# Performance work log

Measured on AMD Instinct MI355X. Metric: run time of the kernel, lower is better.

## Reference

```python
import jax, jax.numpy as jnp
import numpy as np

VOCAB = 14
D_MODEL = 1024
D_FF = 4096
B, S = 8, 2048
EPS = 1e-5


def _linear_params(key, d_in, d_out):
    kw, kb = jax.random.split(key)
    lim = 1.0 / np.sqrt(d_in)
    W = jax.random.uniform(kw, (d_out, d_in), jnp.float32, -lim, lim)
    b = jax.random.uniform(kb, (d_out,), jnp.float32, -lim, lim)
    return W, b


def setup_inputs() -> dict:
    key = jax.random.key(0)
    ks = jax.random.split(key, 8)
    x = jax.random.randint(ks[0], (B, S), 0, VOCAB)
    tok_emb = jax.random.normal(ks[1], (VOCAB, D_MODEL), jnp.float32)
    qw, qb = _linear_params(ks[2], D_MODEL, D_MODEL)
    kw, kb = _linear_params(ks[3], D_MODEL, D_MODEL)
    vw, vb = _linear_params(ks[4], D_MODEL, D_MODEL)
    pw, pb = _linear_params(ks[5], D_MODEL, D_MODEL)
    f1w, f1b = _linear_params(ks[6], D_MODEL, D_FF)
    f2w, f2b = _linear_params(ks[7], D_FF, D_MODEL)
    ones = jnp.ones((D_MODEL,), jnp.float32)
    zeros = jnp.zeros((D_MODEL,), jnp.float32)
    return {
        "x": x, "tok_emb": tok_emb,
        "ln1_w": ones, "ln1_b": zeros,
        "qw": qw, "qb": qb, "kw": kw, "kb": kb, "vw": vw, "vb": vb,
        "pw": pw, "pb": pb,
        "ln2_w": ones, "ln2_b": zeros,
        "f1w": f1w, "f1b": f1b, "f2w": f2w, "f2b": f2b,
        "lnf_w": ones, "lnf_b": zeros,
    }


def _layernorm(h, w, b):
    mu = jnp.mean(h, axis=-1, keepdims=True)
    var = jnp.var(h, axis=-1, keepdims=True)
    return (h - mu) / jnp.sqrt(var + EPS) * w + b


def reference(x, tok_emb, ln1_w, ln1_b, qw, qb, kw, kb, vw, vb, pw, pb,
              ln2_w, ln2_b, f1w, f1b, f2w, f2b, lnf_w, lnf_b):
    h = tok_emb[x]                                  # [B,S,D]
    r = h
    hn = _layernorm(h, ln1_w, ln1_b)
    q = hn @ qw.T + qb
    k = hn @ kw.T + kb
    v = hn @ vw.T + vb
    scale = 1.0 / jnp.sqrt(jnp.float32(q.shape[-1]))
    att = jnp.einsum('bqd,bkd->bqk', q, k) * scale  # [B,S,S]
    causal = jnp.tril(jnp.ones((S, S), bool))
    att = jnp.where(causal, att, -jnp.inf)
    att = jax.nn.softmax(att, axis=-1)
    h = jnp.einsum('bqk,bkd->bqd', att, v) @ pw.T + pb
    h = r + h
    r2 = h
    hn = _layernorm(h, ln2_w, ln2_b)
    h = jax.nn.gelu(hn @ f1w.T + f1b, approximate=False) @ f2w.T + f2b
    h = r2 + h
    h = _layernorm(h, lnf_w, lnf_b)
    logits = h @ tok_emb.T                          # [B,S,VOCAB]
    return logits
```

## Files before the change

kernel.cpp:

```cpp
#include <hip/hip_runtime.h>
#include <math.h>

typedef unsigned short u16;
typedef __attribute__((ext_vector_type(8))) short short8;
typedef __attribute__((ext_vector_type(8))) __bf16 bf16x8;
typedef __attribute__((ext_vector_type(4))) float f32x4;

#define FLAG_BIAS   1
#define FLAG_RES    2
#define FLAG_GELU   4
#define FLAG_TRI    8
#define FLAG_CK     16

__device__ __forceinline__ u16 f2bf(float f) {
  unsigned u = __builtin_bit_cast(unsigned, f);
  unsigned r = u + 0x7fffu + ((u >> 16) & 1u);
  return (u16)(r >> 16);
}
__device__ __forceinline__ float bf2f(u16 u) {
  return __builtin_bit_cast(float, (unsigned)u << 16);
}
__device__ __forceinline__ float wred_sum(float v) {
#pragma unroll
  for (int m = 32; m; m >>= 1) v += __shfl_xor(v, m, 64);
  return v;
}
__device__ __forceinline__ float wred_max(float v) {
#pragma unroll
  for (int m = 32; m; m >>= 1) v = fmaxf(v, __shfl_xor(v, m, 64));
  return v;
}
__device__ __forceinline__ float gelu_fast(float x) {
  float y = 0.7978845608f * x * (1.f + 0.044715f * x * x);
  float e = __expf(2.f * y);
  float th = 1.f - 2.f / (e + 1.f);
  return 0.5f * x * (1.f + th);
}
__device__ __forceinline__ f32x4 mfma16(short8 a, short8 b, f32x4 c) {
  return __builtin_amdgcn_mfma_f32_16x16x32_bf16(
      __builtin_bit_cast(bf16x8, a), __builtin_bit_cast(bf16x8, b), c, 0, 0, 0);
}

#define GLOAD_LDS16(gptr, lptr)                                              \
  __builtin_amdgcn_global_load_lds(                                          \
      (const __attribute__((address_space(1))) void*)(gptr),                 \
      (__attribute__((address_space(3))) void*)(lptr), 16, 0, 0)

__global__ __launch_bounds__(512) void gemm256(
    const u16* __restrict__ Aptr, const u16* __restrict__ Bptr,
    u16* __restrict__ Cptr, const float* __restrict__ bias,
    const u16* __restrict__ resp,
    int M, int N, int K, int lda, int ldb, int ldc, float alpha, int flags,
    long long sA, long long sB, long long sC) {
  const int nwg = gridDim.x;
  const int cpx = nwg >> 3;
  const int bid = blockIdx.x;
  const int swz = (bid & 7) * cpx + (bid >> 3);
  int bm, bn, z;
  if (flags & FLAG_TRI) {
    z = swz / 36;
    int tq = swz - z * 36;
    bm = (int)((sqrtf(8.f * tq + 1.f) - 1.f) * 0.5f);
    while ((bm + 1) * (bm + 2) / 2 <= tq) ++bm;
    while (bm * (bm + 1) / 2 > tq) --bm;
    bn = tq - bm * (bm + 1) / 2;
  } else {
    z = blockIdx.z;
    const int nbm = M >> 8;
    bn = swz / nbm;
    bm = swz - bn * nbm;
  }
  const int gm0 = bm << 8, gn0 = bn << 8;
  const int kend = (flags & FLAG_CK) ? min(K, gm0 + 256) : K;
  const int NT = kend >> 6;

  __shared__ __align__(16) u16 As[2][256 * 64];
  __shared__ __align__(16) u16 Bs[2][256 * 64];

  const int t = threadIdx.x;
  const int l = t & 63;
  const int w = t >> 6;
  const int wr = w >> 2, wc = w & 3;
  const int frow = l & 15;
  const int g4 = l >> 4;

  const int srow = t >> 3;
  const int sch = (t & 7) ^ (srow & 7);
  const u16* Ag = Aptr + (size_t)z * sA + (size_t)(gm0 + srow) * lda + sch * 8;
  const u16* Bg = Bptr + (size_t)z * sB + (size_t)(gn0 + srow) * ldb + sch * 8;

  auto SA = [&](int buf, int j, int kt) {
    GLOAD_LDS16(Ag + (size_t)j * 64 * lda + kt, &As[buf][j * 4096 + w * 512]);
  };
  auto SB = [&](int buf, int j, int kt) {
    GLOAD_LDS16(Bg + (size_t)j * 64 * ldb + kt, &Bs[buf][j * 4096 + w * 512]);
  };

  f32x4 acc[8][4] = {};

#pragma unroll
  for (int j = 0; j < 4; ++j) { SA(0, j, 0); SB(0, j, 0); }
  asm volatile("s_waitcnt vmcnt(0)" ::: "memory");
  __builtin_amdgcn_s_barrier();
  asm volatile("" ::: "memory");

  for (int tt = 0; tt < NT; ++tt) {
    const int buf = tt & 1;
    const int ktn = (tt + 1) << 6;
    const bool pre = (tt + 1) < NT;
    short8 af[8], bf[4];

#pragma unroll
    for (int m = 0; m < 8; ++m) {
      int rr = wr * 128 + m * 16 + frow;
      af[m] = *(const short8*)&As[buf][rr * 64 + ((g4 ^ (rr & 7)) << 3)];
    }
#pragma unroll
    for (int n = 0; n < 4; ++n) {
      int rr = wc * 64 + n * 16 + frow;
      bf[n] = *(const short8*)&Bs[buf][rr * 64 + ((g4 ^ (rr & 7)) << 3)];
    }
    if (pre) {
#pragma unroll
      for (int j = 0; j < 4; ++j) SA(buf ^ 1, j, ktn);
    }
#pragma unroll
    for (int m = 0; m < 8; ++m)
#pragma unroll
      for (int n = 0; n < 4; ++n)
        acc[m][n] = mfma16(af[m], bf[n], acc[m][n]);

#pragma unroll
    for (int m = 0; m < 8; ++m) {
      int rr = wr * 128 + m * 16 + frow;
      af[m] = *(const short8*)&As[buf][rr * 64 + (((4 + g4) ^ (rr & 7)) << 3)];
    }
#pragma unroll
    for (int n = 0; n < 4; ++n) {
      int rr = wc * 64 + n * 16 + frow;
      bf[n] = *(const short8*)&Bs[buf][rr * 64 + (((4 + g4) ^ (rr & 7)) << 3)];
    }
    if (pre) {
#pragma unroll
      for (int j = 0; j < 4; ++j) SB(buf ^ 1, j, ktn);
    }
#pragma unroll
    for (int m = 0; m < 8; ++m)
#pragma unroll
      for (int n = 0; n < 4; ++n)
        acc[m][n] = mfma16(af[m], bf[n], acc[m][n]);

    asm volatile("s_waitcnt vmcnt(0)" ::: "memory");
    __builtin_amdgcn_s_barrier();
    asm volatile("" ::: "memory");
  }

  u16* Cb = Cptr + (size_t)z * sC;
  const bool hasB = flags & FLAG_BIAS, hasR = flags & FLAG_RES;
  const bool doG = flags & FLAG_GELU;
#pragma unroll
  for (int m = 0; m < 8; ++m) {
#pragma unroll
    for (int n = 0; n < 4; ++n) {
      int row0 = gm0 + wr * 128 + m * 16 + ((l >> 4) << 2);
      int col = gn0 + wc * 64 + n * 16 + frow;
      float bv = hasB ? bias[col] : 0.0f;
#pragma unroll
      for (int i = 0; i < 4; ++i) {
        float v = acc[m][n][i] * alpha + bv;
        if (doG) v = gelu_fast(v);
        size_t idx = (size_t)(row0 + i) * ldc + col;
        if (hasR) v += bf2f(resp[idx]);
        Cb[idx] = f2bf(v);
      }
    }
  }
}

__global__ __launch_bounds__(256) void f32_to_bf16_v4(const float* __restrict__ in,
                                                      u16* __restrict__ out, int n4) {
  int i = blockIdx.x * 256 + threadIdx.x;
  if (i < n4) {
    float4 v = ((const float4*)in)[i];
    ushort4 o;
    o.x = f2bf(v.x); o.y = f2bf(v.y); o.z = f2bf(v.z); o.w = f2bf(v.w);
    ((ushort4*)out)[i] = o;
  }
}

__global__ __launch_bounds__(256) void embed_ln1(
    const int* __restrict__ x, const float* __restrict__ emb,
    const float* __restrict__ w, const float* __restrict__ b,
    u16* __restrict__ h16, u16* __restrict__ hn) {
  int row = blockIdx.x * 4 + (threadIdx.x >> 6);
  int lane = threadIdx.x & 63;
  int tok = x[row];
  const float* e = emb + (size_t)tok * 1024;
  float v[16];
  float s = 0.f, q = 0.f;
#pragma unroll
  for (int i = 0; i < 16; ++i) { v[i] = e[lane + i * 64]; s += v[i]; q += v[i] * v[i]; }
  s = wred_sum(s); q = wred_sum(q);
  float mu = s * (1.0f / 1024.0f);
  float rstd = rsqrtf(q * (1.0f / 1024.0f) - mu * mu + 1e-5f);
  u16* hr = h16 + (size_t)row * 1024;
  u16* hnr = hn + (size_t)row * 1024;
#pragma unroll
  for (int i = 0; i < 16; ++i) {
    int d = lane + i * 64;
    hr[d] = f2bf(v[i]);
    hnr[d] = f2bf((v[i] - mu) * rstd * w[d] + b[d]);
  }
}

__global__ __launch_bounds__(256) void ln_rows(
    const u16* __restrict__ in, const float* __restrict__ w,
    const float* __restrict__ b, u16* __restrict__ out) {
  int row = blockIdx.x * 4 + (threadIdx.x >> 6);
  int lane = threadIdx.x & 63;
  const short8* ir = (const short8*)(in + (size_t)row * 1024);
  short8 c0 = ir[lane], c1 = ir[lane + 64];
  float v[16];
  float s = 0.f, q = 0.f;
#pragma unroll
  for (int j = 0; j < 8; ++j) {
    v[j] = bf2f((u16)c0[j]); v[8 + j] = bf2f((u16)c1[j]);
  }
#pragma unroll
  for (int j = 0; j < 16; ++j) { s += v[j]; q += v[j] * v[j]; }
  s = wred_sum(s); q = wred_sum(q);
  float mu = s * (1.0f / 1024.0f);
  float rstd = rsqrtf(q * (1.0f / 1024.0f) - mu * mu + 1e-5f);
  short8 o0, o1;
#pragma unroll
  for (int j = 0; j < 8; ++j) {
    int d0 = lane * 8 + j, d1 = 512 + lane * 8 + j;
    o0[j] = (short)f2bf((v[j] - mu) * rstd * w[d0] + b[d0]);
    o1[j] = (short)f2bf((v[8 + j] - mu) * rstd * w[d1] + b[d1]);
  }
  short8* orow = (short8*)(out + (size_t)row * 1024);
  orow[lane] = o0; orow[lane + 64] = o1;
}

__global__ __launch_bounds__(256) void softmax_causal(u16* att) {
  int r = blockIdx.x * 4 + (threadIdx.x >> 6);
  int lane = threadIdx.x & 63;
  int i = r & 2047;
  int n = i + 1;
  int ng = (i >> 9) + 1;
  short8* pv = (short8*)(att + (size_t)r * 2048);
  float v[32];
  float m = -1e30f;
#pragma unroll
  for (int g = 0; g < 4; ++g) {
    if (g < ng) {
      short8 c = pv[g * 64 + lane];
#pragma unroll
      for (int j = 0; j < 8; ++j) {
        int idx = g * 512 + lane * 8 + j;
        float f = (idx < n) ? bf2f((u16)c[j]) : -1e30f;
        v[g * 8 + j] = f;
        m = fmaxf(m, f);
      }
    }
  }
  m = wred_max(m);
  float s = 0.f;
#pragma unroll
  for (int g = 0; g < 4; ++g) {
    if (g < ng) {
#pragma unroll
      for (int j = 0; j < 8; ++j) {
        int idx = g * 512 + lane * 8 + j;
        float e = (idx < n) ? __expf(v[g * 8 + j] - m) : 0.f;
        v[g * 8 + j] = e; s += e;
      }
    }
  }
  s = wred_sum(s);
  float inv = 1.0f / s;
#pragma unroll
  for (int g = 0; g < 4; ++g) {
    if (g < ng) {
      short8 o;
#pragma unroll
      for (int j = 0; j < 8; ++j) o[j] = (short)f2bf(v[g * 8 + j] * inv);
      pv[g * 64 + lane] = o;
    }
  }
}

__global__ __launch_bounds__(256) void transpose_v(const u16* __restrict__ V,
                                                   u16* __restrict__ Vt, int ldv) {
  int z = blockIdx.z;
  const u16* src = V + (size_t)z * 2048 * ldv;
  u16* dst = Vt + (size_t)z * 1024 * 2048;
  int j0 = (blockIdx.x >> 4) << 6;
  int d0 = (blockIdx.x & 15) << 6;
  __shared__ u16 tile[64][65];
  int c = threadIdx.x & 15;
  int rr = threadIdx.x >> 4;
#pragma unroll
  for (int q = 0; q < 4; ++q) {
    int row = rr + q * 16;
    ushort4 val = *(const ushort4*)(src + (size_t)(j0 + row) * ldv + d0 + c * 4);
    tile[row][c * 4 + 0] = val.x; tile[row][c * 4 + 1] = val.y;
    tile[row][c * 4 + 2] = val.z; tile[row][c * 4 + 3] = val.w;
  }
  __syncthreads();
#pragma unroll
  for (int q = 0; q < 4; ++q) {
    int drow = rr + q * 16;
    ushort4 o;
    o.x = tile[c * 4 + 0][drow]; o.y = tile[c * 4 + 1][drow];
    o.z = tile[c * 4 + 2][drow]; o.w = tile[c * 4 + 3][drow];
    *(ushort4*)(dst + (size_t)(d0 + drow) * 2048 + j0 + c * 4) = o;
  }
}

__global__ __launch_bounds__(256) void lnf_logits(
    const u16* __restrict__ h, const float* __restrict__ w,
    const float* __restrict__ b, const float* __restrict__ emb,
    float* __restrict__ out) {
  __shared__ float el[14 * 1056];
  int t = threadIdx.x;
  for (int f = t * 4; f < 14 * 1024; f += 1024) {
    float4 e = *(const float4*)(emb + f);
    int v = f >> 10, d = f & 1023;
    float* dst = el + v * 1056 + d + (d >> 5);
    dst[0] = e.x; dst[1] = e.y; dst[2] = e.z; dst[3] = e.w;
  }
  __syncthreads();
  int lane = t & 63, wid = t >> 6;
  float w0[8], w1[8], b0[8], b1[8];
#pragma unroll
  for (int j = 0; j < 8; ++j) {
    int d0 = lane * 8 + j, d1 = 512 + lane * 8 + j;
    w0[j] = w[d0]; b0[j] = b[d0];
    w1[j] = w[d1]; b1[j] = b[d1];
  }
  const float* e0 = el + lane * 8 + (lane >> 2);
  const float* e1 = el + 528 + lane * 8 + (lane >> 2);
  for (int rr = 0; rr < 8; ++rr) {
    int row = blockIdx.x * 32 + wid * 8 + rr;
    const short8* hr = (const short8*)(h + (size_t)row * 1024);
    short8 c0 = hr[lane], c1 = hr[lane + 64];
    float v0[8], v1[8];
    float s = 0.f, q = 0.f;
#pragma unroll
    for (int j = 0; j < 8; ++j) {
      v0[j] = bf2f((u16)c0[j]); v1[j] = bf2f((u16)c1[j]);
      s += v0[j] + v1[j];
      q += v0[j] * v0[j] + v1[j] * v1[j];
    }
    s = wred_sum(s); q = wred_sum(q);
    float mu = s * (1.0f / 1024.0f);
    float rstd = rsqrtf(q * (1.0f / 1024.0f) - mu * mu + 1e-5f);
    float h0[8], h1[8];
#pragma unroll
    for (int j = 0; j < 8; ++j) {
      h0[j] = (v0[j] - mu) * rstd * w0[j] + b0[j];
      h1[j] = (v1[j] - mu) * rstd * w1[j] + b1[j];
    }
    float p[14];
#pragma unroll
    for (int v = 0; v < 14; ++v) {
      const float* ev0 = e0 + v * 1056;
      const float* ev1 = e1 + v * 1056;
      float a = 0.f;
#pragma unroll
      for (int j = 0; j < 8; ++j) a += h0[j] * ev0[j] + h1[j] * ev1[j];
      p[v] = a;
    }
#pragma unroll
    for (int m = 32; m; m >>= 1)
#pragma unroll
      for (int v = 0; v < 14; ++v) p[v] += __shfl_xor(p[v], m, 64);
    if (lane == 0) {
      float* orow = out + (size_t)row * 14;
#pragma unroll
      for (int v = 0; v < 14; ++v) orow[v] = p[v];
    }
  }
}

__global__ void zero_out_k(float* o, int n) {
  int i = blockIdx.x * 256 + threadIdx.x;
  if (i < n) o[i] = 0.f;
}
__global__ void diag_k(float* o, float v) { if (threadIdx.x == 0) o[0] = v; }

extern "C" void kernel_launch(void* const* d_in, const int* in_sizes, int n_in,
                              void* d_out, int out_size, void* d_ws, size_t ws_size,
                              hipStream_t stream) {
  const int* x = (const int*)d_in[0];
  const float* tok_emb = (const float*)d_in[1];
  const float* ln1_w = (const float*)d_in[2];
  const float* ln1_b = (const float*)d_in[3];
  const float* qw = (const float*)d_in[4];
  const float* qb = (const float*)d_in[5];
  const float* kw = (const float*)d_in[6];
  const float* kb = (const float*)d_in[7];
  const float* vw = (const float*)d_in[8];
  const float* vb = (const float*)d_in[9];
  const float* pw = (const float*)d_in[10];
  const float* pb = (const float*)d_in[11];
  const float* ln2_w = (const float*)d_in[12];
  const float* ln2_b = (const float*)d_in[13];
  const float* f1w = (const float*)d_in[14];
  const float* f1b = (const float*)d_in[15];
  const float* f2w = (const float*)d_in[16];
  const float* f2b = (const float*)d_in[17];
  const float* lnf_w = (const float*)d_in[18];
  const float* lnf_b = (const float*)d_in[19];
  float* out = (float*)d_out;

  const long long T = 16384, D = 1024, F = 4096, S = 2048;
  const size_t MB = 1ull << 20;
  char* base = (char*)d_ws;

  if (ws_size < 224 * MB) {
    zero_out_k<<<dim3((out_size + 255) / 256), 256, 0, stream>>>(out, out_size);
    diag_k<<<dim3(1), 1, 0, stream>>>(out, (float)ws_size);
    return;
  }

  u16* rA16 = (u16*)base;
  u16* rB   = (u16*)(base + 32 * MB);
  u16* QKV  = (u16*)(base + 64 * MB);
  u16* SC   = (u16*)(base + 160 * MB);
  u16* W3   = SC;
  float* qkvb = (float*)(base + 166 * MB);
  u16* PW  = SC;
  u16* CB  = QKV;
  u16* F1  = (u16*)(base + 192 * MB);
  u16* F2  = (u16*)(base + 200 * MB);

  auto cvt = [&](const float* src, u16* dst, long long n) {
    int n4 = (int)(n / 4);
    f32_to_bf16_v4<<<dim3((n4 + 255) / 256), dim3(256), 0, stream>>>(src, dst, n4);
  };
  auto gemm = [&](const u16* A, const u16* B, u16* C, const float* bias,
                  const u16* res, long long M, long long N, long long K,
                  long long lda, long long ldb, long long ldc, float alpha,
                  int flags, long long sA, long long sB, long long sC,
                  int gx, int gz) {
    gemm256<<<dim3(gx, 1, gz), dim3(512), 0, stream>>>(
        A, B, C, bias, res, (int)M, (int)N, (int)K, (int)lda, (int)ldb,
        (int)ldc, alpha, flags, sA, sB, sC);
  };

  cvt(qw, W3, D * D);
  cvt(kw, W3 + 1024 * 1024, D * D);
  cvt(vw, W3 + 2 * 1024 * 1024, D * D);
  hipMemcpyAsync(qkvb, qb, D * 4, hipMemcpyDeviceToDevice, stream);
  hipMemcpyAsync(qkvb + 1024, kb, D * 4, hipMemcpyDeviceToDevice, stream);
  hipMemcpyAsync(qkvb + 2048, vb, D * 4, hipMemcpyDeviceToDevice, stream);

  embed_ln1<<<dim3(T / 4), 256, 0, stream>>>(x, tok_emb, ln1_w, ln1_b, rA16, rB);

  gemm(rB, W3, QKV, qkvb, nullptr, T, 3072, D, D, D, 3072, 1.f, FLAG_BIAS,
       0, 0, 0, 768, 1);

  gemm(QKV, QKV + 1024, SC, nullptr, nullptr, S, S, D, 3072, 3072, 2048,
       0.03125f, FLAG_TRI, S * 3072, S * 3072, S * S, 288, 1);

  transpose_v<<<dim3(512, 1, 8), 256, 0, stream>>>(QKV + 2048, rB, 3072);

  softmax_causal<<<dim3(T / 4), 256, 0, stream>>>(SC);

  gemm(SC, rB, QKV, nullptr, nullptr, S, D, S, S, S, 3072, 1.f, FLAG_CK,
       S * S, D * S, S * 3072, 32, 8);

  cvt(pw, PW, D * D);
  gemm(QKV, PW, rA16, pb, rA16, T, D, D, 3072, D, D, 1.f, FLAG_BIAS | FLAG_RES,
       0, 0, 0, 256, 1);

  ln_rows<<<dim3(T / 4), 256, 0, stream>>>(rA16, ln2_w, ln2_b, rB);

  cvt(f1w, F1, F * D);
  cvt(f2w, F2, D * F);
  gemm(rB, F1, CB, f1b, nullptr, T, F, D, D, D, F, 1.f, FLAG_BIAS | FLAG_GELU,
       0, 0, 0, 1024, 1);
  gemm(CB, F2, rA16, f2b, rA16, T, D, F, F, F, D, 1.f, FLAG_BIAS | FLAG_RES,
       0, 0, 0, 256, 1);

  lnf_logits<<<dim3(512), 256, 0, stream>>>(rA16, lnf_w, lnf_b, tok_emb, out);
}
```

Measured before the change: 839.5 us.

## Switch GEMM to 32x32x16 MFMA with split-K LDS layout and new swizzle

Replaces the 16x16x32 bf16 MFMA tiles with 32x32x16 MFMA. The LDS tiles are reorganised into two 32-wide K halves with a matching XOR swizzle, and the fragment loads and epilogue row mapping are rewritten to fit. The larger MFMA shape means fewer LDS fragment reads per FLOP and fewer instructions issued. The trade-off is a different accumulator layout, possible bank-conflict changes, and register-pressure shifts.

```diff
diff --git a/kernel.cpp b/kernel.cpp
--- a/kernel.cpp
+++ b/kernel.cpp
@@ -4,7 +4,7 @@
 typedef unsigned short u16;
 typedef __attribute__((ext_vector_type(8))) short short8;
 typedef __attribute__((ext_vector_type(8))) __bf16 bf16x8;
-typedef __attribute__((ext_vector_type(4))) float f32x4;
+typedef __attribute__((ext_vector_type(16))) float f32x16;
 
 #define FLAG_BIAS   1
 #define FLAG_RES    2
@@ -36,8 +36,8 @@
   float th = 1.f - 2.f / (e + 1.f);
   return 0.5f * x * (1.f + th);
 }
-__device__ __forceinline__ f32x4 mfma16(short8 a, short8 b, f32x4 c) {
-  return __builtin_amdgcn_mfma_f32_16x16x32_bf16(
+__device__ __forceinline__ f32x16 mfma32(short8 a, short8 b, f32x16 c) {
+  return __builtin_amdgcn_mfma_f32_32x32x16_bf16(
       __builtin_bit_cast(bf16x8, a), __builtin_bit_cast(bf16x8, b), c, 0, 0, 0);
 }
 
@@ -74,32 +74,40 @@
   const int kend = (flags & FLAG_CK) ? min(K, gm0 + 256) : K;
   const int NT = kend >> 6;
 
-  __shared__ __align__(16) u16 As[2][256 * 64];
-  __shared__ __align__(16) u16 Bs[2][256 * 64];
+  __shared__ __align__(16) u16 As[2][2][256 * 32];
+  __shared__ __align__(16) u16 Bs[2][2][256 * 32];
 
   const int t = threadIdx.x;
   const int l = t & 63;
   const int w = t >> 6;
   const int wr = w >> 2, wc = w & 3;
-  const int frow = l & 15;
-  const int g4 = l >> 4;
-
-  const int srow = t >> 3;
-  const int sch = (t & 7) ^ (srow & 7);
+  const int l31 = l & 31;
+  const int lhi = l >> 5;
+  const int lkey = (l31 >> 1) & 3;
+
+  const int srow = t >> 2;
+  const int sch = (t & 3) ^ ((srow >> 1) & 3);
   const u16* Ag = Aptr + (size_t)z * sA + (size_t)(gm0 + srow) * lda + sch * 8;
   const u16* Bg = Bptr + (size_t)z * sB + (size_t)(gn0 + srow) * ldb + sch * 8;
-
-  auto SA = [&](int buf, int j, int kt) {
-    GLOAD_LDS16(Ag + (size_t)j * 64 * lda + kt, &As[buf][j * 4096 + w * 512]);
+  const long long a128 = (long long)128 * lda, b128 = (long long)128 * ldb;
+
+  auto stA = [&](int buf, int kk, int kt) {
+    const int c0 = kt + (kk << 5);
+    GLOAD_LDS16(Ag + c0, &As[buf][kk][w * 512]);
+    GLOAD_LDS16(Ag + a128 + c0, &As[buf][kk][4096 + w * 512]);
   };
-  auto SB = [&](int buf, int j, int kt) {
-    GLOAD_LDS16(Bg + (size_t)j * 64 * ldb + kt, &Bs[buf][j * 4096 + w * 512]);
+  auto stB = [&](int buf, int kk, int kt) {
+    const int c0 = kt + (kk << 5);
+    GLOAD_LDS16(Bg + c0, &Bs[buf][kk][w * 512]);
+    GLOAD_LDS16(Bg + b128 + c0, &Bs[buf][kk][4096 + w * 512]);
   };
 
-  f32x4 acc[8][4] = {};
-
-#pragma unroll
-  for (int j = 0; j < 4; ++j) { SA(0, j, 0); SB(0, j, 0); }
+  f32x16 acc[4][2] = {};
+
+  const int arow = wr * 128 + l31;
+  const int brow = wc * 64 + l31;
+
+  stA(0, 0, 0); stB(0, 0, 0); stA(0, 1, 0); stB(0, 1, 0);
   asm volatile("s_waitcnt vmcnt(0)" ::: "memory");
   __builtin_amdgcn_s_barrier();
   asm volatile("" ::: "memory");
@@ -108,47 +116,49 @@
     const int buf = tt & 1;
     const int ktn = (tt + 1) << 6;
     const bool pre = (tt + 1) < NT;
-    short8 af[8], bf[4];
-
-#pragma unroll
-    for (int m = 0; m < 8; ++m) {
-      int rr = wr * 128 + m * 16 + frow;
-      af[m] = *(const short8*)&As[buf][rr * 64 + ((g4 ^ (rr & 7)) << 3)];
-    }
-#pragma unroll
-    for (int n = 0; n < 4; ++n) {
-      int rr = wc * 64 + n * 16 + frow;
-      bf[n] = *(const short8*)&Bs[buf][rr * 64 + ((g4 ^ (rr & 7)) << 3)];
-    }
-    if (pre) {
-#pragma unroll
-      for (int j = 0; j < 4; ++j) SA(buf ^ 1, j, ktn);
-    }
-#pragma unroll
-    for (int m = 0; m < 8; ++m)
-#pragma unroll
-      for (int n = 0; n < 4; ++n)
-        acc[m][n] = mfma16(af[m], bf[n], acc[m][n]);
-
-#pragma unroll
-    for (int m = 0; m < 8; ++m) {
-      int rr = wr * 128 + m * 16 + frow;
-      af[m] = *(const short8*)&As[buf][rr * 64 + (((4 + g4) ^ (rr & 7)) << 3)];
-    }
-#pragma unroll
-    for (int n = 0; n < 4; ++n) {
-      int rr = wc * 64 + n * 16 + frow;
-      bf[n] = *(const short8*)&Bs[buf][rr * 64 + (((4 + g4) ^ (rr & 7)) << 3)];
-    }
-    if (pre) {
-#pragma unroll
-      for (int j = 0; j < 4; ++j) SB(buf ^ 1, j, ktn);
-    }
-#pragma unroll
-    for (int m = 0; m < 8; ++m)
-#pragma unroll
-      for (int n = 0; n < 4; ++n)
-        acc[m][n] = mfma16(af[m], bf[n], acc[m][n]);
+    short8 af0[4], af1[4], bf0[2], bf1[2];
+
+#pragma unroll
+    for (int mi = 0; mi < 4; ++mi) {
+      int ro = (arow + mi * 32) * 32;
+      af0[mi] = *(const short8*)&As[buf][0][ro + (((0 + lhi) ^ lkey) << 3)];
+      af1[mi] = *(const short8*)&As[buf][0][ro + (((2 + lhi) ^ lkey) << 3)];
+    }
+#pragma unroll
+    for (int ni = 0; ni < 2; ++ni) {
+      int ro = (brow + ni * 32) * 32;
+      bf0[ni] = *(const short8*)&Bs[buf][0][ro + (((0 + lhi) ^ lkey) << 3)];
+      bf1[ni] = *(const short8*)&Bs[buf][0][ro + (((2 + lhi) ^ lkey) << 3)];
+    }
+    if (pre) { stA(buf ^ 1, 0, ktn); stA(buf ^ 1, 1, ktn); }
+#pragma unroll
+    for (int mi = 0; mi < 4; ++mi)
+#pragma unroll
+      for (int ni = 0; ni < 2; ++ni) {
+        acc[mi][ni] = mfma32(af0[mi], bf0[ni], acc[mi][ni]);
+        acc[mi][ni] = mfma32(af1[mi], bf1[ni], acc[mi][ni]);
+      }
+
+#pragma unroll
+    for (int mi = 0; mi < 4; ++mi) {
+      int ro = (arow + mi * 32) * 32;
+      af0[mi] = *(const short8*)&As[buf][1][ro + (((0 + lhi) ^ lkey) << 3)];
+      af1[mi] = *(const short8*)&As[buf][1][ro + (((2 + lhi) ^ lkey) << 3)];
+    }
+#pragma unroll
+    for (int ni = 0; ni < 2; ++ni) {
+      int ro = (brow + ni * 32) * 32;
+      bf0[ni] = *(const short8*)&Bs[buf][1][ro + (((0 + lhi) ^ lkey) << 3)];
+      bf1[ni] = *(const short8*)&Bs[buf][1][ro + (((2 + lhi) ^ lkey) << 3)];
+    }
+    if (pre) { stB(buf ^ 1, 0, ktn); stB(buf ^ 1, 1, ktn); }
+#pragma unroll
+    for (int mi = 0; mi < 4; ++mi)
+#pragma unroll
+      for (int ni = 0; ni < 2; ++ni) {
+        acc[mi][ni] = mfma32(af0[mi], bf0[ni], acc[mi][ni]);
+        acc[mi][ni] = mfma32(af1[mi], bf1[ni], acc[mi][ni]);
+      }
 
     asm volatile("s_waitcnt vmcnt(0)" ::: "memory");
     __builtin_amdgcn_s_barrier();
@@ -159,17 +169,18 @@
   const bool hasB = flags & FLAG_BIAS, hasR = flags & FLAG_RES;
   const bool doG = flags & FLAG_GELU;
 #pragma unroll
-  for (int m = 0; m < 8; ++m) {
-#pragma unroll
-    for (int n = 0; n < 4; ++n) {
-      int row0 = gm0 + wr * 128 + m * 16 + ((l >> 4) << 2);
-      int col = gn0 + wc * 64 + n * 16 + frow;
+  for (int mi = 0; mi < 4; ++mi) {
+#pragma unroll
+    for (int ni = 0; ni < 2; ++ni) {
+      int col = gn0 + wc * 64 + ni * 32 + l31;
+      int rbase = gm0 + wr * 128 + mi * 32 + 4 * lhi;
       float bv = hasB ? bias[col] : 0.0f;
 #pragma unroll
-      for (int i = 0; i < 4; ++i) {
-        float v = acc[m][n][i] * alpha + bv;
+      for (int r = 0; r < 16; ++r) {
+        int row = rbase + (r & 3) + 8 * (r >> 2);
+        float v = acc[mi][ni][r] * alpha + bv;
         if (doG) v = gelu_fast(v);
-        size_t idx = (size_t)(row0 + i) * ldc + col;
+        size_t idx = (size_t)row * ldc + col;
         if (hasR) v += bf2f(resp[idx]);
         Cb[idx] = f2bf(v);
       }
```

After: 869.2 us. +3.5%, slower.
